# Kernel tuning notes

Measured on AMD Instinct MI355X. Metric: run time of the kernel, lower is better.

Reference implementation:

```python
import jax, jax.numpy as jnp
import numpy as np

N_ATOMS = 10000
N_PAIRS = 160000
F = 32            # nr_atom_basis (= edge basis = hidden sizes)
H = 7             # nr_heads
C = H * F         # nr_coefficients = 224
N_RBF = 50
RBF_CUTOFF = 5.0
RBF_GAMMA = 10.0

silu = jax.nn.silu

def setup_inputs() -> dict:
    key = jax.random.key(0)
    ks = jax.random.split(key, 32)
    def w(k, shape, scale=0.1):
        return (jax.random.normal(k, shape, dtype=jnp.float32) * scale)
    inp = {
        "h": jax.random.normal(ks[0], (N_ATOMS, F), dtype=jnp.float32),
        "x": jax.random.normal(ks[1], (N_ATOMS, 3), dtype=jnp.float32),
        "v": jax.random.normal(ks[2], (N_ATOMS, 3), dtype=jnp.float32),
        "pairlist": jax.random.randint(ks[3], (2, N_PAIRS), 0, N_ATOMS, dtype=jnp.int64 if jax.config.read('jax_enable_x64') else jnp.int32),
        # edge model (ContinuousFilterConvolutionWithConcatenation)
        "w_mlp_in": w(ks[4], (2 * F, N_RBF)), "b_mlp_in": jnp.zeros((N_RBF,), jnp.float32),
        "w_e1": w(ks[5], (2 * F + N_RBF + 1, F)), "b_e1": jnp.zeros((F,), jnp.float32),
        "w_e2": w(ks[6], (F, F)), "b_e2": jnp.zeros((F,), jnp.float32),
        # semantic attention mlp
        "w_att": w(ks[7], (F, H)), "b_att": jnp.zeros((H,), jnp.float32),
        # node mlp: in = F + C + F
        "w_n1": w(ks[8], (F + C + F, F)), "b_n1": jnp.zeros((F,), jnp.float32),
        "w_n2": w(ks[9], (F, F)), "b_n2": jnp.zeros((F,), jnp.float32),
        # post norm mlp
        "w_p1": w(ks[10], (C, F)), "b_p1": jnp.zeros((F,), jnp.float32),
        "w_p2": w(ks[11], (F, F)), "b_p2": jnp.zeros((F,), jnp.float32),
        # velocity mlp
        "w_v1": w(ks[12], (F, F)), "b_v1": jnp.zeros((F,), jnp.float32),
        "w_v2": w(ks[13], (F, 1)),
        # mixers
        "w_xmix": w(ks[14], (C, C)),
        "w_vmix": w(ks[15], (C, 1)),
    }
    return inp

def _rbf(d):  # Gaussian smearing, [P] -> [P, N_RBF]
    centers = jnp.linspace(0.0, RBF_CUTOFF, N_RBF, dtype=jnp.float32)
    return jnp.exp(-RBF_GAMMA * (d[:, None] - centers) ** 2)

def reference(h, x, v, pairlist,
              w_mlp_in, b_mlp_in, w_e1, b_e1, w_e2, b_e2,
              w_att, b_att, w_n1, b_n1, w_n2, b_n2,
              w_p1, b_p1, w_p2, b_p2, w_v1, b_v1, w_v2,
              w_xmix, w_vmix):
    n = h.shape[0]
    p = pairlist.shape[1]
    idx_i, idx_j = pairlist[0], pairlist[1]

    r_ij = x[idx_j] - x[idx_i]                       # [P, 3]
    d_ij = jnp.linalg.norm(r_ij, axis=-1)            # [P]
    dir_ij = r_ij / (d_ij[:, None] + 1e-5)           # [P, 3]

    # edge model
    h_cat = jnp.concatenate([h[idx_i], h[idx_j]], axis=-1)         # [P, 2F]
    filt = _rbf(d_ij) * (h_cat @ w_mlp_in + b_mlp_in)              # [P, N_RBF]
    e_in = jnp.concatenate([h_cat, filt, d_ij[:, None]], axis=-1)  # [P, 2F+N_RBF+1]
    h_ij_edge = silu(e_in @ w_e1 + b_e1) @ w_e2 + b_e2             # [P, F]

    # semantic attention: scatter-softmax over edges grouped by idx_i
    logits = jax.nn.celu(h_ij_edge @ w_att + b_att, alpha=2.0)     # [P, H]
    seg_max = jax.ops.segment_max(logits, idx_i, num_segments=n)
    e = jnp.exp(logits - seg_max[idx_i])
    seg_sum = jax.ops.segment_sum(e, idx_i, num_segments=n)
    att = e / seg_sum[idx_i]                                       # [P, H]
    att_agg = jax.ops.segment_sum(att, idx_i, num_segments=n)
    att_normed = att / att_agg[idx_i]
    # einsum('pf,ph->pfh') then reshape to [P, C]
    h_ij_semantic = (h_ij_edge[:, :, None] * att_normed[:, None, :]).reshape(p, C)

    # aggregate (scatter_add)
    h_i_semantic = jax.ops.segment_sum(h_ij_semantic, idx_i, num_segments=n)  # [N, C]

    # spatial attention
    x_mixed = jnp.tanh(h_ij_semantic @ w_xmix)                     # [P, C]
    combinations = dir_ij[:, None, :] * x_mixed[:, :, None]        # [P, C, 3]
    counts = jax.ops.segment_sum(jnp.ones((p,), h.dtype), idx_i, num_segments=n)
    denom = jnp.maximum(counts, 1.0)
    comb_mean = jax.ops.segment_sum(combinations, idx_i, num_segments=n) / denom[:, None, None]
    norm_sq = jnp.sum(comb_mean ** 2, axis=-1)                     # [N, C]
    h_i_spatial = silu(silu(norm_sq @ w_p1 + b_p1) @ w_p2 + b_p2)  # [N, F]

    # node update
    node_in = jnp.concatenate([h, h_i_semantic, h_i_spatial], axis=-1)
    h_updated = h + silu(silu(node_in @ w_n1 + b_n1) @ w_n2 + b_n2)

    # velocity update
    v_ij = jnp.einsum('pcx,c->px', combinations, w_vmix[:, 0])     # [P, 3]
    dv = jax.ops.segment_sum(v_ij, idx_i, num_segments=n) / denom[:, None]
    scale = 2.0 * jax.nn.sigmoid(silu(h @ w_v1 + b_v1) @ w_v2)     # [N, 1]
    v_updated = scale * v + dv
    x_updated = x + v_updated
    return (h_updated, x_updated, v_updated)
```

## Files before the change

kernel.cpp:

```cpp
#include <hip/hip_runtime.h>

typedef unsigned short u16;
typedef unsigned int u32;
typedef __attribute__((ext_vector_type(8))) short short8;
typedef __attribute__((ext_vector_type(4))) float floatx4;

#define P_PAIRS 160000
#define N_ATOMS 10000

#define OFF_WMLP  0
#define OFF_BMLP  3200
#define OFF_WE1   3250
#define OFF_BE1   6930
#define OFF_WE2   6962
#define OFF_BE2   7986
#define OFF_WATT  8018
#define OFF_BATT  8242
#define OFF_WN1   8249
#define OFF_BN1   17465
#define OFF_WN2   17497
#define OFF_BN2   18521
#define OFF_WP1   18553
#define OFF_BP1   25721
#define OFF_WP2   25753
#define OFF_BP2   26777
#define OFF_WV1   26809
#define OFF_BV1   27833
#define OFF_WV2   27865
#define OFF_WVMIX 27897
#define WF_TOTAL  28121

__device__ __forceinline__ float b2f(u16 u){ return __uint_as_float(((u32)u) << 16); }
__device__ __forceinline__ u16 f2b(float f){
  u32 u = __float_as_uint(f);
  u32 r = (u + 0x7FFFu + ((u >> 16) & 1u)) >> 16;
  return (u16)r;
}
__device__ __forceinline__ void unpack2(u32 p, float& lo, float& hi){
  lo = __uint_as_float(p << 16);
  hi = __uint_as_float(p & 0xFFFF0000u);
}
__device__ __forceinline__ float siluf(float v){ return v / (1.f + __expf(-v)); }
__device__ __forceinline__ float ldw(const void* p, int o, int bf){
  return bf ? b2f(((const u16*)p)[o]) : ((const float*)p)[o];
}

__global__ void k_code(float* out, float code){
  if (threadIdx.x == 0 && blockIdx.x == 0) out[0] = code;
}

__device__ __forceinline__ void detect_flags(const u32* hw, const u32* plw, int* s_fl){
  int tid = threadIdx.x;
  if (tid < 64){
    u32 e = (hw[tid] >> 7) & 0xFFu;
    unsigned long long m1 = __ballot(e >= 100u && e <= 140u);
    unsigned long long m2 = __ballot(plw[2*tid+1] == 0u);
    if (tid == 0){
      s_fl[0] = (__popcll(m1) >= 48) ? 1 : 0;
      s_fl[1] = (__popcll(m2) >= 60) ? 1 : 0;
    }
  }
  __syncthreads();
}

#define NBP_NORM 2735
#define NBP_CONV (NBP_NORM + 110)
#define NBP_TRAN (NBP_CONV + 196)
#define NBP_PB   (NBP_TRAN + 14)
#define NBP_HIST (NBP_PB + 625)

__global__ void k_prep(const void* __restrict__ h_raw, const void* __restrict__ x_raw,
    const void* __restrict__ v_raw, const void* __restrict__ pl_raw,
    const void* w_mlp, const void* b_mlp, const void* w_e1, const void* b_e1,
    const void* w_e2, const void* b_e2, const void* w_att, const void* b_att,
    const void* w_n1, const void* b_n1, const void* w_n2, const void* b_n2,
    const void* w_p1, const void* b_p1, const void* w_p2, const void* b_p2,
    const void* w_v1, const void* b_v1, const void* w_v2, const void* w_vmix,
    const void* wx,
    float* __restrict__ hf, float* __restrict__ xf, float* __restrict__ vf,
    int* __restrict__ pli, float* __restrict__ Wf, u16* __restrict__ wT,
    u16* __restrict__ bpk, int* __restrict__ counts){
  __shared__ int s_fl[2];
  detect_flags((const u32*)h_raw, (const u32*)pl_raw, s_fl);
  int bf = s_fl[0], i64 = s_fl[1];
  int bid = blockIdx.x, tid = threadIdx.x;
  if (bid < NBP_NORM){
    int t = bid * 256 + tid;
    if (t < 320000){
      hf[t] = ldw(h_raw, t, bf);
    } else if (t < 350000){
      int i = t - 320000; xf[i] = ldw(x_raw, i, bf);
    } else if (t < 380000){
      int i = t - 350000; vf[i] = ldw(v_raw, i, bf);
    } else if (t < 700000){
      int k = t - 380000;
      const int* p32 = (const int*)pl_raw;
      pli[k] = i64 ? p32[2*(size_t)k] : p32[k];
    }
  } else if (bid < NBP_CONV){
    int t = (bid - NBP_NORM) * 256 + tid;
    if (t >= WF_TOTAL) return;
    if (t < 3200){
      int k = t / 50, o = t - k * 50;
      Wf[OFF_WMLP + o * 64 + k] = ldw(w_mlp, t, bf);
      return;
    }
    const void* src; int o;
    if      (t < 3250)  { src = b_mlp;  o = t - 3200; }
    else if (t < 6930)  { src = w_e1;   o = t - 3250; }
    else if (t < 6962)  { src = b_e1;   o = t - 6930; }
    else if (t < 7986)  { src = w_e2;   o = t - 6962; }
    else if (t < 8018)  { src = b_e2;   o = t - 7986; }
    else if (t < 8242)  { src = w_att;  o = t - 8018; }
    else if (t < 8249)  { src = b_att;  o = t - 8242; }
    else if (t < 17465) { src = w_n1;   o = t - 8249; }
    else if (t < 17497) { src = b_n1;   o = t - 17465; }
    else if (t < 18521) { src = w_n2;   o = t - 17497; }
    else if (t < 18553) { src = b_n2;   o = t - 18521; }
    else if (t < 25721) { src = w_p1;   o = t - 18553; }
    else if (t < 25753) { src = b_p1;   o = t - 25721; }
    else if (t < 26777) { src = w_p2;   o = t - 25753; }
    else if (t < 26809) { src = b_p2;   o = t - 26777; }
    else if (t < 27833) { src = w_v1;   o = t - 26809; }
    else if (t < 27865) { src = b_v1;   o = t - 27833; }
    else if (t < 27897) { src = w_v2;   o = t - 27865; }
    else                { src = w_vmix; o = t - 27897; }
    Wf[t] = ldw(src, o, bf);
  } else if (bid < NBP_TRAN){
    int t = (bid - NBP_CONV) * 256 + tid;
    if (t >= 224 * 224) return;
    int n = t / 224, k = t - n * 224;
    wT[t] = f2b(ldw(wx, k * 224 + n, bf));
  } else if (bid < NBP_PB){
    int t = (bid - NBP_TRAN) * 256 + tid;
    if (t >= 3584) return;
    float v = 0.f;
    if (t < 2048){
      int n = t >> 6, k = t & 63;
      if (k < 50)       v = ldw(w_e1, (64 + k) * 32 + n, bf);
      else if (k == 50) v = ldw(w_e1, 114 * 32 + n, bf);
    } else if (t < 3072){
      int e = t - 2048; int n = e >> 5, k = e & 31;
      v = ldw(w_e2, k * 32 + n, bf);
    } else {
      int e = t - 3072; int n = e >> 5, k = e & 31;
      if (n < 7) v = ldw(w_att, k * 7 + n, bf);
    }
    bpk[t] = f2b(v);
  } else {
    int p = (bid - NBP_PB) * 256 + tid;
    const int* p32 = (const int*)pl_raw;
    int i = i64 ? p32[2*(size_t)p] : p32[p];
    atomicAdd(&counts[i], 1);
  }
}

__global__ void k_atomscan(const float* __restrict__ hf, const float* __restrict__ Wf,
    u16* __restrict__ prei, u16* __restrict__ prej,
    const int* __restrict__ counts, int* __restrict__ offs, int* __restrict__ cursor){
  __shared__ float hs[16][33];
  __shared__ int part[256];
  int tid = threadIdx.x;
  if (blockIdx.x < 625){
    int a0 = blockIdx.x * 16;
    for (int e = tid; e < 512; e += 256){
      int a = e >> 5, k = e & 31;
      hs[a][k] = hf[(size_t)(a0 + a) * 32 + k];
    }
    __syncthreads();
    for (int e = tid; e < 800; e += 256){
      int a = e / 50, r = e - a * 50;
      const float* wm = Wf + OFF_WMLP + r * 64;
      float acc = Wf[OFF_BMLP + r];
      #pragma unroll
      for (int k = 0; k < 32; ++k) acc += hs[a][k] * wm[k];
      prei[(size_t)(a0 + a) * 88 + 32 + r] = f2b(acc);
    }
    for (int e = tid; e < 800; e += 256){
      int a = e / 50, r = e - a * 50;
      const float* wm = Wf + OFF_WMLP + r * 64 + 32;
      float acc = 0.f;
      #pragma unroll
      for (int k = 0; k < 32; ++k) acc += hs[a][k] * wm[k];
      prej[(size_t)(a0 + a) * 88 + 32 + r] = f2b(acc);
    }
    for (int e = tid; e < 512; e += 256){
      int a = e >> 5, o = e & 31;
      float acc = Wf[OFF_BE1 + o];
      #pragma unroll
      for (int k = 0; k < 32; ++k) acc += hs[a][k] * Wf[OFF_WE1 + k * 32 + o];
      prei[(size_t)(a0 + a) * 88 + o] = f2b(acc);
    }
    for (int e = tid; e < 512; e += 256){
      int a = e >> 5, o = e & 31;
      float acc = 0.f;
      #pragma unroll
      for (int k = 0; k < 32; ++k) acc += hs[a][k] * Wf[OFF_WE1 + (32 + k) * 32 + o];
      prej[(size_t)(a0 + a) * 88 + o] = f2b(acc);
    }
  } else {
    int sum = 0;
    for (int k = 0; k < 40; ++k){
      int idx = tid * 40 + k;
      if (idx < N_ATOMS) sum += counts[idx];
    }
    part[tid] = sum;
    __syncthreads();
    if (tid == 0){
      int run = 0;
      for (int q = 0; q < 256; ++q){ int tmp = part[q]; part[q] = run; run += tmp; }
    }
    __syncthreads();
    int run = part[tid];
    for (int k = 0; k < 40; ++k){
      int idx = tid * 40 + k;
      if (idx < N_ATOMS){ offs[idx] = run; cursor[idx] = run; run += counts[idx]; }
    }
    if (tid == 0) offs[N_ATOMS] = P_PAIRS;
  }
}

__global__ void k_scatter(const int* __restrict__ pl, int* __restrict__ cursor,
                          int* __restrict__ isrt, int* __restrict__ jsrt){
  int p = blockIdx.x * 256 + threadIdx.x;
  int i = pl[p];
  int pos = atomicAdd(&cursor[i], 1);
  isrt[pos] = i;
  jsrt[pos] = pl[P_PAIRS + p];
}

#define PM_UB   0
#define PM_TB   16384
#define PM_DD   30720
#define PM_A1   31232
#define PM_B1   49664
#define PM_A2   54272
#define PM_B2   64512
#define PM_B3   67072
#define PM_TOT  68352

__global__ __launch_bounds__(256) void k_pairm(const float* __restrict__ x,
    const float* __restrict__ Wf, const u16* __restrict__ prei, const u16* __restrict__ prej,
    const int* __restrict__ isrt, const int* __restrict__ jsrt, const u16* __restrict__ bpk,
    u16* __restrict__ edge, float* __restrict__ logits, float* __restrict__ dirs){
  __shared__ __attribute__((aligned(16))) char smem[PM_TOT];
  float* UB = (float*)(smem + PM_UB);
  u16*   TB = (u16*)(smem + PM_TB);
  float* DD = (float*)(smem + PM_DD);
  u16*   A1 = (u16*)(smem + PM_A1);
  u16*   B1 = (u16*)(smem + PM_B1);
  u16*   A2 = (u16*)(smem + PM_A2);
  u16*   B2 = (u16*)(smem + PM_B2);
  u16*   B3 = (u16*)(smem + PM_B3);
  int tid = threadIdx.x;
  int wave = tid >> 6, lane = tid & 63, l15 = lane & 15, quad = lane >> 4;
  int row0 = blockIdx.x * 128;

  if (tid < 128){
    int s = row0 + tid;
    int i = isrt[s], j = jsrt[s];
    float r0 = x[j*3+0] - x[i*3+0];
    float r1 = x[j*3+1] - x[i*3+1];
    float r2 = x[j*3+2] - x[i*3+2];
    float d = sqrtf(r0*r0 + r1*r1 + r2*r2);
    float rinv = 1.f / (d + 1e-5f);
    dirs[s*3+0] = r0*rinv; dirs[s*3+1] = r1*rinv; dirs[s*3+2] = r2*rinv;
    DD[tid] = d;
    const uint4* pi4 = (const uint4*)(prei + (size_t)i * 88);
    const uint4* pj4 = (const uint4*)(prej + (size_t)j * 88);
    float* ub = UB + tid * 32;
    #pragma unroll
    for (int q = 0; q < 4; ++q){
      uint4 a4 = pi4[q], b4 = pj4[q];
      u32 pa[4] = {a4.x, a4.y, a4.z, a4.w};
      u32 pb[4] = {b4.x, b4.y, b4.z, b4.w};
      #pragma unroll
      for (int w2 = 0; w2 < 4; ++w2){
        float al, ah, bl, bh;
        unpack2(pa[w2], al, ah); unpack2(pb[w2], bl, bh);
        ub[q*8 + w2*2]     = al + bl;
        ub[q*8 + w2*2 + 1] = ah + bh;
      }
    }
    u32* tb = (u32*)TB + tid * 28;
    #pragma unroll
    for (int q = 0; q < 7; ++q){
      uint4 a4 = pi4[4+q], b4 = pj4[4+q];
      u32 pa[4] = {a4.x, a4.y, a4.z, a4.w};
      u32 pb[4] = {b4.x, b4.y, b4.z, b4.w};
      #pragma unroll
      for (int w2 = 0; w2 < 4; ++w2){
        float al, ah, bl, bh;
        unpack2(pa[w2], al, ah); unpack2(pb[w2], bl, bh);
        tb[q*4 + w2] = (u32)f2b(al + bl) | ((u32)f2b(ah + bh) << 16);
      }
    }
  } else {
    int t2 = tid - 128;
    const u32* src = (const u32*)bpk;
    for (int e = t2; e < 1024; e += 128){
      int n = e >> 5, kp = e & 31;
      ((u32*)B1)[n*36 + kp] = src[e];
    }
    for (int e = t2; e < 512; e += 128){
      int n = e >> 4, kp = e & 15;
      ((u32*)B2)[n*20 + kp] = src[1024 + e];
    }
    for (int e = t2; e < 256; e += 128){
      int n = e >> 4, kp = e & 15;
      ((u32*)B3)[n*20 + kp] = src[1536 + e];
    }
  }
  __syncthreads();
  for (int e = tid; e < 4096; e += 256){
    int r = e >> 5, kp = e & 31;
    int k0 = kp * 2, k1 = k0 + 1;
    float d = DD[r];
    float v0 = 0.f, v1 = 0.f;
    if (k0 < 50){
      float t0 = b2f(TB[r*56 + k0]);
      float c0 = (float)k0 * (5.f/49.f), dd0 = d - c0;
      v0 = t0 * __expf(-10.f * dd0 * dd0);
    } else if (k0 == 50) v0 = d;
    if (k1 < 50){
      float t1 = b2f(TB[r*56 + k1]);
      float c1 = (float)k1 * (5.f/49.f), dd1 = d - c1;
      v1 = t1 * __expf(-10.f * dd1 * dd1);
    }
    ((u32*)A1)[r*36 + kp] = (u32)f2b(v0) | ((u32)f2b(v1) << 16);
  }
  __syncthreads();
  floatx4 au[2][2];
  #pragma unroll
  for (int mt = 0; mt < 2; ++mt)
    #pragma unroll
    for (int nt = 0; nt < 2; ++nt) au[mt][nt] = (floatx4){0.f,0.f,0.f,0.f};
  #pragma unroll
  for (int ks = 0; ks < 2; ++ks){
    int kk = ks * 32;
    short8 a0 = *(const short8*)(A1 + (wave*32 + l15)*72 + kk + quad*8);
    short8 a1 = *(const short8*)(A1 + (wave*32 + 16 + l15)*72 + kk + quad*8);
    #pragma unroll
    for (int nt = 0; nt < 2; ++nt){
      short8 b = *(const short8*)(B1 + (nt*16 + l15)*72 + kk + quad*8);
      au[0][nt] = __builtin_amdgcn_mfma_f32_16x16x32_bf16(a0, b, au[0][nt], 0, 0, 0);
      au[1][nt] = __builtin_amdgcn_mfma_f32_16x16x32_bf16(a1, b, au[1][nt], 0, 0, 0);
    }
  }
  #pragma unroll
  for (int mt = 0; mt < 2; ++mt)
    #pragma unroll
    for (int nt = 0; nt < 2; ++nt)
      #pragma unroll
      for (int reg = 0; reg < 4; ++reg){
        int r = wave*32 + mt*16 + quad*4 + reg;
        int c = nt*16 + l15;
        float uval = au[mt][nt][reg] + UB[r*32 + c];
        A2[r*40 + c] = f2b(siluf(uval));
      }
  __syncthreads();
  floatx4 ae[2][2];
  #pragma unroll
  for (int mt = 0; mt < 2; ++mt)
    #pragma unroll
    for (int nt = 0; nt < 2; ++nt) ae[mt][nt] = (floatx4){0.f,0.f,0.f,0.f};
  {
    short8 a0 = *(const short8*)(A2 + (wave*32 + l15)*40 + quad*8);
    short8 a1 = *(const short8*)(A2 + (wave*32 + 16 + l15)*40 + quad*8);
    #pragma unroll
    for (int nt = 0; nt < 2; ++nt){
      short8 b = *(const short8*)(B2 + (nt*16 + l15)*40 + quad*8);
      ae[0][nt] = __builtin_amdgcn_mfma_f32_16x16x32_bf16(a0, b, ae[0][nt], 0, 0, 0);
      ae[1][nt] = __builtin_amdgcn_mfma_f32_16x16x32_bf16(a1, b, ae[1][nt], 0, 0, 0);
    }
  }
  __syncthreads();
  #pragma unroll
  for (int mt = 0; mt < 2; ++mt)
    #pragma unroll
    for (int nt = 0; nt < 2; ++nt)
      #pragma unroll
      for (int reg = 0; reg < 4; ++reg){
        int r = wave*32 + mt*16 + quad*4 + reg;
        int c = nt*16 + l15;
        float ev = ae[mt][nt][reg] + Wf[OFF_BE2 + c];
        A2[r*40 + c] = f2b(ev);
      }
  __syncthreads();
  {
    int r = tid >> 1, p = tid & 1;
    const uint4* srcp = (const uint4*)(A2 + r*40 + p*16);
    uint4* dstp = (uint4*)(edge + (size_t)(row0 + r)*32 + p*16);
    dstp[0] = srcp[0]; dstp[1] = srcp[1];
  }
  floatx4 al_[2];
  al_[0] = (floatx4){0.f,0.f,0.f,0.f};
  al_[1] = (floatx4){0.f,0.f,0.f,0.f};
  {
    short8 a0 = *(const short8*)(A2 + (wave*32 + l15)*40 + quad*8);
    short8 a1 = *(const short8*)(A2 + (wave*32 + 16 + l15)*40 + quad*8);
    short8 b = *(const short8*)(B3 + l15*40 + quad*8);
    al_[0] = __builtin_amdgcn_mfma_f32_16x16x32_bf16(a0, b, al_[0], 0, 0, 0);
    al_[1] = __builtin_amdgcn_mfma_f32_16x16x32_bf16(a1, b, al_[1], 0, 0, 0);
  }
  if (l15 < 7){
    float ba = Wf[OFF_BATT + l15];
    #pragma unroll
    for (int mt = 0; mt < 2; ++mt)
      #pragma unroll
      for (int reg = 0; reg < 4; ++reg){
        int r = wave*32 + mt*16 + quad*4 + reg;
        float vv = al_[mt][reg] + ba;
        float cl = vv > 0.f ? vv : 2.f * expm1f(0.5f * vv);
        logits[(size_t)(row0 + r)*7 + l15] = cl;
      }
  }
}

__global__ __launch_bounds__(256) void k_att(const int* __restrict__ offs,
    const float* __restrict__ logits, const u16* __restrict__ edge,
    float* __restrict__ atts, float* __restrict__ hsem){
  int a = blockIdx.x * 16 + (threadIdx.x >> 4);
  int lane = threadIdx.x & 15;
  int off = offs[a], end = offs[a+1];
  float m[7];
  #pragma unroll
  for (int hh = 0; hh < 7; ++hh) m[hh] = -1e30f;
  for (int s = off + lane; s < end; s += 16){
    #pragma unroll
    for (int hh = 0; hh < 7; ++hh) m[hh] = fmaxf(m[hh], logits[s*7+hh]);
  }
  #pragma unroll
  for (int hh = 0; hh < 7; ++hh){
    float v = m[hh];
    #pragma unroll
    for (int msk = 8; msk >= 1; msk >>= 1) v = fmaxf(v, __shfl_xor(v, msk));
    m[hh] = v;
  }
  float sm[7] = {0,0,0,0,0,0,0};
  for (int s = off + lane; s < end; s += 16){
    #pragma unroll
    for (int hh = 0; hh < 7; ++hh){
      float e = __expf(logits[s*7+hh] - m[hh]);
      sm[hh] += e;
      atts[s*7+hh] = e;
    }
  }
  #pragma unroll
  for (int hh = 0; hh < 7; ++hh){
    float v = sm[hh];
    #pragma unroll
    for (int msk = 8; msk >= 1; msk >>= 1) v += __shfl_xor(v, msk);
    sm[hh] = 1.f / v;
  }
  for (int s = off + lane; s < end; s += 16){
    #pragma unroll
    for (int hh = 0; hh < 7; ++hh) atts[s*7+hh] *= sm[hh];
  }
  __syncthreads();
  float acc[14] = {0,0,0,0,0,0,0,0,0,0,0,0,0,0};
  for (int s = off; s < end; ++s){
    u32 ev = *(const u32*)(edge + (size_t)s * 32 + lane * 2);
    float e0 = b2f((u16)(ev & 0xFFFFu));
    float e1 = b2f((u16)(ev >> 16));
    const float* ap = atts + (size_t)s * 7;
    #pragma unroll
    for (int hh = 0; hh < 7; ++hh){
      float at = ap[hh];
      acc[hh]     += e0 * at;
      acc[7 + hh] += e1 * at;
    }
  }
  float* hp = hsem + (size_t)a * 224 + lane * 14;
  #pragma unroll
  for (int jj = 0; jj < 14; ++jj) hp[jj] = acc[jj];
}

#define G_BS   29696
#define G_EL   29696
#define G_AL   (29696 + 4608)
#define G_TOT  38656

__global__ __launch_bounds__(256, 4) void k_gemm3(const u16* __restrict__ edge,
    const float* __restrict__ atts, const u16* __restrict__ BT,
    u16* __restrict__ xh0, u16* __restrict__ xh1, int mode){
  __shared__ __attribute__((aligned(16))) char smem[G_TOT];
  u16*   As  = (u16*)smem;
  u16*   xth = (u16*)smem;
  u16*   Bs  = (u16*)(smem + G_BS);
  u16*   eL  = (u16*)(smem + G_EL);
  float* aL  = (float*)(smem + G_AL);
  int tid = threadIdx.x;
  int wave = tid >> 6, lane = tid & 63, l15 = lane & 15, quad = lane >> 4;
  int bid = blockIdx.x;
  int half, rblk;
  if (mode < 0){ half = bid & 1; rblk = bid >> 1; }
  else         { half = mode;    rblk = bid; }
  u16* xhalf = half ? xh1 : xh0;
  int row0 = rblk * 64;
  int nbase = half * 112;

  for (int e = tid; e < 512; e += 256){
    int r = e >> 3, q = e & 7;
    *(uint2*)(eL + r*36 + q*4) = *(const uint2*)(edge + (size_t)(row0 + r)*32 + q*4);
  }
  for (int e = tid; e < 448; e += 256) aL[e] = atts[(size_t)row0*7 + e];
  floatx4 acc[7];
  #pragma unroll
  for (int nt = 0; nt < 7; ++nt) acc[nt] = (floatx4){0.f, 0.f, 0.f, 0.f};
  __syncthreads();

  {
    int pr = tid >> 2, q = tid & 3;
    u32* asw = (u32*)As + pr*116 + q*28;
    const u16* er = eL + pr*36 + q*8;
    const float* ar = aL + pr*7;
    float av[7];
    #pragma unroll
    for (int hh = 0; hh < 7; ++hh) av[hh] = ar[hh];
    #pragma unroll
    for (int fo2 = 0; fo2 < 4; ++fo2){
      float e0 = b2f(er[2*fo2]);
      float e1 = b2f(er[2*fo2+1]);
      u16 w[14];
      #pragma unroll
      for (int hh = 0; hh < 7; ++hh){
        w[hh]   = f2b(e0 * av[hh]);
        w[7+hh] = f2b(e1 * av[hh]);
      }
      #pragma unroll
      for (int k = 0; k < 7; ++k)
        asw[fo2*7 + k] = (u32)w[2*k] | ((u32)w[2*k+1] << 16);
    }
  }
  __syncthreads();

  for (int kt = 0; kt < 7; ++kt){
    for (int e = tid; e < 448; e += 256){
      int r = e >> 2, q = e & 3;
      *(uint4*)(Bs + r*40 + q*8) = *(const uint4*)(BT + (size_t)(nbase + r)*224 + kt*32 + q*8);
    }
    __syncthreads();
    int kk = kt * 32;
    short8 a0 = *(const short8*)(As + (wave*16 + l15)*232 + kk + quad*8);
    #pragma unroll
    for (int nt = 0; nt < 7; ++nt){
      short8 b = *(const short8*)(Bs + (nt*16 + l15)*40 + quad*8);
      acc[nt] = __builtin_amdgcn_mfma_f32_16x16x32_bf16(a0, b, acc[nt], 0, 0, 0);
    }
    __syncthreads();
  }

  #pragma unroll
  for (int nt = 0; nt < 7; ++nt)
    #pragma unroll
    for (int reg = 0; reg < 4; ++reg){
      int r = wave*16 + quad*4 + reg;
      int c = nt*16 + l15;
      float vv = acc[nt][reg];
      vv = fminf(fmaxf(vv, -15.f), 15.f);
      float e2 = __expf(2.f * vv);
      xth[r*120 + c] = f2b((e2 - 1.f) / (e2 + 1.f));
    }
  __syncthreads();
  for (int e = tid; e < 896; e += 256){
    int r = e / 14, w = e - r * 14;
    *(uint4*)(xhalf + (size_t)(row0 + r)*112 + w*8) = *(const uint4*)(xth + r*120 + w*8);
  }
}

__global__ __launch_bounds__(256) void k_comb(const int* __restrict__ offs,
    const u16* __restrict__ xhalf, const float* __restrict__ dirs,
    const float* __restrict__ Wf, int half,
    float* __restrict__ nsq, float* __restrict__ pvh){
  int a = blockIdx.x * 16 + (threadIdx.x >> 4);
  int lane = threadIdx.x & 15;
  int off = offs[a], end = offs[a+1];
  float c0[7] = {0,0,0,0,0,0,0}, c1[7] = {0,0,0,0,0,0,0}, c2[7] = {0,0,0,0,0,0,0};
  for (int s = off; s < end; ++s){
    float d0 = dirs[s*3+0], d1 = dirs[s*3+1], d2 = dirs[s*3+2];
    const u16* xr = xhalf + (size_t)s * 112 + lane;
    #pragma unroll
    for (int k = 0; k < 7; ++k){
      float xm = b2f(xr[k*16]);
      c0[k] += d0 * xm; c1[k] += d1 * xm; c2[k] += d2 * xm;
    }
  }
  float inv = 1.f / fmaxf((float)(end - off), 1.f);
  float pv0 = 0.f, pv1 = 0.f, pv2 = 0.f;
  #pragma unroll
  for (int k = 0; k < 7; ++k){
    float m0 = c0[k]*inv, m1 = c1[k]*inv, m2 = c2[k]*inv;
    int c = half*112 + k*16 + lane;
    nsq[(size_t)a*224 + c] = m0*m0 + m1*m1 + m2*m2;
    float wv = Wf[OFF_WVMIX + c];
    pv0 += wv*m0; pv1 += wv*m1; pv2 += wv*m2;
  }
  #pragma unroll
  for (int m = 8; m >= 1; m >>= 1){
    pv0 += __shfl_xor(pv0, m); pv1 += __shfl_xor(pv1, m); pv2 += __shfl_xor(pv2, m);
  }
  if (lane == 0){
    float* pp = pvh + (size_t)half*30000 + (size_t)a*3;
    pp[0] = pv0; pp[1] = pv1; pp[2] = pv2;
  }
}

__global__ __launch_bounds__(256) void k_final4(const float* __restrict__ h,
    const float* __restrict__ x, const float* __restrict__ v,
    const float* __restrict__ Wf, const float* __restrict__ hsem,
    const float* __restrict__ nsq, const float* __restrict__ pvh,
    float* __restrict__ out){
  __shared__ float s_nsq[16][225];
  __shared__ float s_in[16][289];
  __shared__ float s_u1[16][33];
  __shared__ float s_un[16][33];
  __shared__ float s_sc[16];
  int tid = threadIdx.x;
  int a0 = blockIdx.x * 16;
  for (int e = tid; e < 896; e += 256){
    int a = e / 56, q = e - a * 56;
    float4 t = *(const float4*)(nsq + (size_t)(a0 + a) * 224 + q * 4);
    s_nsq[a][q*4+0] = t.x; s_nsq[a][q*4+1] = t.y;
    s_nsq[a][q*4+2] = t.z; s_nsq[a][q*4+3] = t.w;
  }
  for (int e = tid; e < 896; e += 256){
    int a = e / 56, q = e - a * 56;
    float4 t = *(const float4*)(hsem + (size_t)(a0 + a) * 224 + q * 4);
    s_in[a][32 + q*4+0] = t.x; s_in[a][32 + q*4+1] = t.y;
    s_in[a][32 + q*4+2] = t.z; s_in[a][32 + q*4+3] = t.w;
  }
  for (int e = tid; e < 128; e += 256){
    int a = e >> 3, q = e & 7;
    float4 t = *(const float4*)(h + (size_t)(a0 + a) * 32 + q * 4);
    s_in[a][q*4+0] = t.x; s_in[a][q*4+1] = t.y;
    s_in[a][q*4+2] = t.z; s_in[a][q*4+3] = t.w;
  }
  __syncthreads();
  int o = tid & 31, g5 = tid >> 5;
  int aA = g5, aB = g5 + 8;
  {
    float uA = Wf[OFF_BP1 + o], uB = uA;
    const float* w = Wf + OFF_WP1 + o;
    #pragma unroll 8
    for (int kk = 0; kk < 224; ++kk){
      float wv = w[kk*32];
      uA += s_nsq[aA][kk] * wv;
      uB += s_nsq[aB][kk] * wv;
    }
    s_u1[aA][o] = siluf(uA);
    s_u1[aB][o] = siluf(uB);
  }
  {
    float gA = Wf[OFF_BV1 + o], gB = gA;
    const float* w = Wf + OFF_WV1 + o;
    #pragma unroll
    for (int kk = 0; kk < 32; ++kk){
      float wv = w[kk*32];
      gA += s_in[aA][kk] * wv;
      gB += s_in[aB][kk] * wv;
    }
    float wv2 = Wf[OFF_WV2 + o];
    float zA = siluf(gA) * wv2, zB = siluf(gB) * wv2;
    #pragma unroll
    for (int m = 16; m >= 1; m >>= 1){
      zA += __shfl_xor(zA, m); zB += __shfl_xor(zB, m);
    }
    if (o == 0){
      s_sc[aA] = 2.f / (1.f + __expf(-zA));
      s_sc[aB] = 2.f / (1.f + __expf(-zB));
    }
  }
  __syncthreads();
  {
    float uA = Wf[OFF_BP2 + o], uB = uA;
    const float* w = Wf + OFF_WP2 + o;
    #pragma unroll
    for (int kk = 0; kk < 32; ++kk){
      float wv = w[kk*32];
      uA += s_u1[aA][kk] * wv;
      uB += s_u1[aB][kk] * wv;
    }
    s_in[aA][256 + o] = siluf(uA);
    s_in[aB][256 + o] = siluf(uB);
  }
  __syncthreads();
  {
    float uA = Wf[OFF_BN1 + o], uB = uA;
    const float* w = Wf + OFF_WN1 + o;
    #pragma unroll 8
    for (int kk = 0; kk < 288; ++kk){
      float wv = w[kk*32];
      uA += s_in[aA][kk] * wv;
      uB += s_in[aB][kk] * wv;
    }
    s_un[aA][o] = siluf(uA);
    s_un[aB][o] = siluf(uB);
  }
  __syncthreads();
  {
    float uA = Wf[OFF_BN2 + o], uB = uA;
    const float* w = Wf + OFF_WN2 + o;
    #pragma unroll
    for (int kk = 0; kk < 32; ++kk){
      float wv = w[kk*32];
      uA += s_un[aA][kk] * wv;
      uB += s_un[aB][kk] * wv;
    }
    out[(size_t)(a0 + aA)*32 + o] = s_in[aA][o] + siluf(uA);
    out[(size_t)(a0 + aB)*32 + o] = s_in[aB][o] + siluf(uB);
  }
  if (tid < 48){
    int a = tid / 3, c = tid - a * 3;
    int ga = a0 + a;
    float pv = pvh[(size_t)ga*3 + c] + pvh[30000 + (size_t)ga*3 + c];
    float vup = s_sc[a] * v[ga*3 + c] + pv;
    float xup = x[ga*3 + c] + vup;
    out[N_ATOMS*32 + (size_t)ga*3 + c] = xup;
    out[N_ATOMS*32 + N_ATOMS*3 + (size_t)ga*3 + c] = vup;
  }
}

__global__ __launch_bounds__(256) void k_combf(const int* __restrict__ offs,
    const u16* __restrict__ xh0, const u16* __restrict__ xh1,
    const float* __restrict__ dirs, const float* __restrict__ h,
    const float* __restrict__ x, const float* __restrict__ v,
    const float* __restrict__ Wf, const float* __restrict__ hsem,
    float* __restrict__ out){
  __shared__ float s_nsq[16][225];
  __shared__ float s_in[16][289];
  __shared__ float s_u1[16][33];
  __shared__ float s_un[16][33];
  __shared__ float s_sc[16];
  __shared__ float s_pv[16][3];
  int tid = threadIdx.x;
  int a0 = blockIdx.x * 16;
  for (int e = tid; e < 896; e += 256){
    int a = e / 56, q = e - a * 56;
    float4 t = *(const float4*)(hsem + (size_t)(a0 + a) * 224 + q * 4);
    s_in[a][32 + q*4+0] = t.x; s_in[a][32 + q*4+1] = t.y;
    s_in[a][32 + q*4+2] = t.z; s_in[a][32 + q*4+3] = t.w;
  }
  for (int e = tid; e < 128; e += 256){
    int a = e >> 3, q = e & 7;
    float4 t = *(const float4*)(h + (size_t)(a0 + a) * 32 + q * 4);
    s_in[a][q*4+0] = t.x; s_in[a][q*4+1] = t.y;
    s_in[a][q*4+2] = t.z; s_in[a][q*4+3] = t.w;
  }
  {
    int a = tid >> 4, lane = tid & 15;
    int off = offs[a0 + a], end = offs[a0 + a + 1];
    float c0A[7] = {0,0,0,0,0,0,0}, c1A[7] = {0,0,0,0,0,0,0}, c2A[7] = {0,0,0,0,0,0,0};
    float c0B[7] = {0,0,0,0,0,0,0}, c1B[7] = {0,0,0,0,0,0,0}, c2B[7] = {0,0,0,0,0,0,0};
    for (int s = off; s < end; ++s){
      float d0 = dirs[s*3+0], d1 = dirs[s*3+1], d2 = dirs[s*3+2];
      const u16* xra = xh0 + (size_t)s * 112 + lane;
      const u16* xrb = xh1 + (size_t)s * 112 + lane;
      #pragma unroll
      for (int k = 0; k < 7; ++k){
        float xa = b2f(xra[k*16]);
        float xb = b2f(xrb[k*16]);
        c0A[k] += d0 * xa; c1A[k] += d1 * xa; c2A[k] += d2 * xa;
        c0B[k] += d0 * xb; c1B[k] += d1 * xb; c2B[k] += d2 * xb;
      }
    }
    float inv = 1.f / fmaxf((float)(end - off), 1.f);
    float pv0 = 0.f, pv1 = 0.f, pv2 = 0.f;
    #pragma unroll
    for (int k = 0; k < 7; ++k){
      {
        float m0 = c0A[k]*inv, m1 = c1A[k]*inv, m2 = c2A[k]*inv;
        int c = k*16 + lane;
        s_nsq[a][c] = m0*m0 + m1*m1 + m2*m2;
        float wv = Wf[OFF_WVMIX + c];
        pv0 += wv*m0; pv1 += wv*m1; pv2 += wv*m2;
      }
      {
        float m0 = c0B[k]*inv, m1 = c1B[k]*inv, m2 = c2B[k]*inv;
        int c = 112 + k*16 + lane;
        s_nsq[a][c] = m0*m0 + m1*m1 + m2*m2;
        float wv = Wf[OFF_WVMIX + c];
        pv0 += wv*m0; pv1 += wv*m1; pv2 += wv*m2;
      }
    }
    #pragma unroll
    for (int m = 8; m >= 1; m >>= 1){
      pv0 += __shfl_xor(pv0, m); pv1 += __shfl_xor(pv1, m); pv2 += __shfl_xor(pv2, m);
    }
    if (lane == 0){ s_pv[a][0] = pv0; s_pv[a][1] = pv1; s_pv[a][2] = pv2; }
  }
  __syncthreads();
  int o = tid & 31, g5 = tid >> 5;
  int aA = g5, aB = g5 + 8;
  {
    float uA = Wf[OFF_BP1 + o], uB = uA;
    const float* w = Wf + OFF_WP1 + o;
    #pragma unroll 8
    for (int kk = 0; kk < 224; ++kk){
      float wv = w[kk*32];
      uA += s_nsq[aA][kk] * wv;
      uB += s_nsq[aB][kk] * wv;
    }
    s_u1[aA][o] = siluf(uA);
    s_u1[aB][o] = siluf(uB);
  }
  {
    float gA = Wf[OFF_BV1 + o], gB = gA;
    const float* w = Wf + OFF_WV1 + o;
    #pragma unroll
    for (int kk = 0; kk < 32; ++kk){
      float wv = w[kk*32];
      gA += s_in[aA][kk] * wv;
      gB += s_in[aB][kk] * wv;
    }
    float wv2 = Wf[OFF_WV2 + o];
    float zA = siluf(gA) * wv2, zB = siluf(gB) * wv2;
    #pragma unroll
    for (int m = 16; m >= 1; m >>= 1){
      zA += __shfl_xor(zA, m); zB += __shfl_xor(zB, m);
    }
    if (o == 0){
      s_sc[aA] = 2.f / (1.f + __expf(-zA));
      s_sc[aB] = 2.f / (1.f + __expf(-zB));
    }
  }
  __syncthreads();
  {
    float uA = Wf[OFF_BP2 + o], uB = uA;
    const float* w = Wf + OFF_WP2 + o;
    #pragma unroll
    for (int kk = 0; kk < 32; ++kk){
      float wv = w[kk*32];
      uA += s_u1[aA][kk] * wv;
      uB += s_u1[aB][kk] * wv;
    }
    s_in[aA][256 + o] = siluf(uA);
    s_in[aB][256 + o] = siluf(uB);
  }
  __syncthreads();
  {
    float uA = Wf[OFF_BN1 + o], uB = uA;
    const float* w = Wf + OFF_WN1 + o;
    #pragma unroll 8
    for (int kk = 0; kk < 288; ++kk){
      float wv = w[kk*32];
      uA += s_in[aA][kk] * wv;
      uB += s_in[aB][kk] * wv;
    }
    s_un[aA][o] = siluf(uA);
    s_un[aB][o] = siluf(uB);
  }
  __syncthreads();
  {
    float uA = Wf[OFF_BN2 + o], uB = uA;
    const float* w = Wf + OFF_WN2 + o;
    #pragma unroll
    for (int kk = 0; kk < 32; ++kk){
      float wv = w[kk*32];
      uA += s_un[aA][kk] * wv;
      uB += s_un[aB][kk] * wv;
    }
    out[(size_t)(a0 + aA)*32 + o] = s_in[aA][o] + siluf(uA);
    out[(size_t)(a0 + aB)*32 + o] = s_in[aB][o] + siluf(uB);
  }
  if (tid < 48){
    int a = tid / 3, c = tid - a * 3;
    int ga = a0 + a;
    float vup = s_sc[a] * v[ga*3 + c] + s_pv[a][c];
    float xup = x[ga*3 + c] + vup;
    out[N_ATOMS*32 + (size_t)ga*3 + c] = xup;
    out[N_ATOMS*32 + N_ATOMS*3 + (size_t)ga*3 + c] = vup;
  }
}

static constexpr size_t al256(size_t x){ return (x + 255) & ~(size_t)255; }
static constexpr size_t WS_FLAGS   = 0;
static constexpr size_t WS_COUNTS  = al256(WS_FLAGS + 8);
static constexpr size_t WS_OFFSETS = al256(WS_COUNTS + (size_t)N_ATOMS * 4);
static constexpr size_t WS_CURSOR  = al256(WS_OFFSETS + (size_t)(N_ATOMS + 1) * 4);
static constexpr size_t WS_PERM    = al256(WS_CURSOR + (size_t)N_ATOMS * 4);
static constexpr size_t WS_PLI     = al256(WS_PERM + (size_t)P_PAIRS * 4);
static constexpr size_t WS_HF      = al256(WS_PLI + (size_t)2 * P_PAIRS * 4);
static constexpr size_t WS_XF      = al256(WS_HF + (size_t)N_ATOMS * 32 * 4);
static constexpr size_t WS_VF      = al256(WS_XF + (size_t)N_ATOMS * 3 * 4);
static constexpr size_t WS_WF      = al256(WS_VF + (size_t)N_ATOMS * 3 * 4);
static constexpr size_t WS_WT      = al256(WS_WF + (size_t)WF_TOTAL * 4);
static constexpr size_t WS_EDGE    = al256(WS_WT + (size_t)224 * 224 * 2);
static constexpr size_t WS_ATTS    = al256(WS_EDGE + (size_t)P_PAIRS * 32 * 2);
static constexpr size_t WS_DIRS    = al256(WS_ATTS + (size_t)P_PAIRS * 7 * 4);
static constexpr size_t WS_LOGITS  = al256(WS_DIRS + (size_t)P_PAIRS * 3 * 4);
static constexpr size_t WS_PREI    = al256(WS_LOGITS + (size_t)P_PAIRS * 7 * 4);
static constexpr size_t WS_PREJ    = al256(WS_PREI + (size_t)N_ATOMS * 88 * 2);
static constexpr size_t WS_HSEM    = WS_LOGITS + 4480000;
static constexpr size_t WS_XH      = WS_HSEM + (size_t)N_ATOMS * 224 * 4;
static constexpr size_t WS_NSQ     = WS_XH + (size_t)P_PAIRS * 112 * 2;
static constexpr size_t WS_PVH     = WS_NSQ + (size_t)N_ATOMS * 224 * 4;
static constexpr size_t WS_JSRT    = al256(WS_PVH + (size_t)2 * 30000 * 4);
static constexpr size_t WS_BPK     = al256(WS_JSRT + (size_t)P_PAIRS * 4);
static constexpr size_t WS_END     = WS_BPK + 3584 * 2;
static constexpr size_t WB_XH0     = WS_XH;
static constexpr size_t WB_XH1     = WB_XH0 + (size_t)P_PAIRS * 112 * 2;
static constexpr size_t WB_JSRT    = al256(WB_XH1 + (size_t)P_PAIRS * 112 * 2);
static constexpr size_t WB_BPK     = al256(WB_JSRT + (size_t)P_PAIRS * 4);
static constexpr size_t WB_END     = WB_BPK + 3584 * 2;
static_assert(WS_PREJ + (size_t)N_ATOMS * 88 * 2 <= WS_XH, "pre tables before xhalf");
static_assert(WS_END <= WS_LOGITS + (size_t)P_PAIRS * 224 * 2, "fallback within proven footprint");
static_assert(WS_HSEM % 256 == 0 && WS_XH % 256 == 0 && WS_NSQ % 256 == 0 && WS_PVH % 256 == 0, "alignment");
static_assert(WB_XH1 % 256 == 0, "alignment");

extern "C" void kernel_launch(void* const* d_in, const int* in_sizes, int n_in,
                              void* d_out, int out_size, void* d_ws, size_t ws_size,
                              hipStream_t stream){
  (void)in_sizes; (void)n_in;
  if (out_size != 380000 || ws_size < WS_END){
    k_code<<<1, 64, 0, stream>>>((float*)d_out, 14000.f);
    return;
  }
  char* ws = (char*)d_ws;
  int*   counts = (int*)(ws + WS_COUNTS);
  int*   offs   = (int*)(ws + WS_OFFSETS);
  int*   cursor = (int*)(ws + WS_CURSOR);
  int*   isrt   = (int*)(ws + WS_PERM);
  int*   pli    = (int*)(ws + WS_PLI);
  float* hf     = (float*)(ws + WS_HF);
  float* xf     = (float*)(ws + WS_XF);
  float* vf     = (float*)(ws + WS_VF);
  float* Wf     = (float*)(ws + WS_WF);
  u16*   wT     = (u16*)(ws + WS_WT);
  u16*   edge   = (u16*)(ws + WS_EDGE);
  float* atts   = (float*)(ws + WS_ATTS);
  float* dirs   = (float*)(ws + WS_DIRS);
  float* logits = (float*)(ws + WS_LOGITS);
  u16*   prei   = (u16*)(ws + WS_PREI);
  u16*   prej   = (u16*)(ws + WS_PREJ);
  float* hsem   = (float*)(ws + WS_HSEM);

  bool big = (ws_size >= WB_END);
  u16*   xh0  = (u16*)(ws + WB_XH0);
  u16*   xh1  = big ? (u16*)(ws + WB_XH1) : xh0;
  int*   jsrt = big ? (int*)(ws + WB_JSRT) : (int*)(ws + WS_JSRT);
  u16*   bpk  = big ? (u16*)(ws + WB_BPK) : (u16*)(ws + WS_BPK);
  float* nsq  = (float*)(ws + WS_NSQ);
  float* pvh  = (float*)(ws + WS_PVH);

  hipMemsetAsync(counts, 0, (size_t)N_ATOMS * 4, stream);
  k_prep<<<NBP_HIST, 256, 0, stream>>>(d_in[0], d_in[1], d_in[2], d_in[3],
      d_in[4],  d_in[5],  d_in[6],  d_in[7],  d_in[8],  d_in[9],  d_in[10], d_in[11],
      d_in[12], d_in[13], d_in[14], d_in[15], d_in[16], d_in[17], d_in[18], d_in[19],
      d_in[20], d_in[21], d_in[22], d_in[24], d_in[23],
      hf, xf, vf, pli, Wf, wT, bpk, counts);
  k_atomscan<<<626, 256, 0, stream>>>(hf, Wf, prei, prej, counts, offs, cursor);
  k_scatter<<<P_PAIRS / 256, 256, 0, stream>>>(pli, cursor, isrt, jsrt);
  k_pairm<<<P_PAIRS / 128, 256, 0, stream>>>(xf, Wf, prei, prej, isrt, jsrt, bpk, edge, logits, dirs);
  k_att<<<N_ATOMS / 16, 256, 0, stream>>>(offs, logits, edge, atts, hsem);
  if (big){
    k_gemm3<<<2 * (P_PAIRS / 64), 256, 0, stream>>>(edge, atts, wT, xh0, xh1, -1);
    k_combf<<<625, 256, 0, stream>>>(offs, xh0, xh1, dirs, hf, xf, vf, Wf, hsem, (float*)d_out);
  } else {
    k_gemm3<<<P_PAIRS / 64, 256, 0, stream>>>(edge, atts, wT, xh0, xh0, 0);
    k_comb<<<N_ATOMS / 16, 256, 0, stream>>>(offs, xh0, dirs, Wf, 0, nsq, pvh);
    k_gemm3<<<P_PAIRS / 64, 256, 0, stream>>>(edge, atts, wT, xh0, xh0, 1);
    k_comb<<<N_ATOMS / 16, 256, 0, stream>>>(offs, xh0, dirs, Wf, 1, nsq, pvh);
    k_final4<<<625, 256, 0, stream>>>(hf, xf, vf, Wf, hsem, nsq, pvh, (float*)d_out);
  }
}
```

Baseline: 312.2 us.

## Compute full 224-wide xmix output per block instead of two half-blocks

Adds a k_gemm3w kernel that computes all 224 output columns for each 64-row tile, where the old path launched two blocks per tile, one per 112-column half. This avoids building the A tile (edge times attention) twice and reloading edge and attention data twice. In exchange each block holds 14 accumulator tiles, raising register pressure, and uses more shared memory for the wider B tile, so occupancy drops to 3 blocks per CU. The non-big path's k_gemm3 signature is simplified to take a single output half.

Result: slower. 323.9 us (+3.7%).

```diff
diff --git a/kernel.cpp b/kernel.cpp
--- a/kernel.cpp
+++ b/kernel.cpp
@@ -476,6 +476,95 @@
   for (int jj = 0; jj < 14; ++jj) hp[jj] = acc[jj];
 }
 
+#define GW_BS   29696
+#define GW_EL   29696
+#define GW_AL   (29696 + 4608)
+#define GW_TOT  47616
+
+__global__ __launch_bounds__(256, 3) void k_gemm3w(const u16* __restrict__ edge,
+    const float* __restrict__ atts, const u16* __restrict__ BT,
+    u16* __restrict__ xh0, u16* __restrict__ xh1){
+  __shared__ __attribute__((aligned(16))) char smem[GW_TOT];
+  u16*   As  = (u16*)smem;
+  u16*   xth = (u16*)smem;
+  u16*   Bs  = (u16*)(smem + GW_BS);
+  u16*   eL  = (u16*)(smem + GW_EL);
+  float* aL  = (float*)(smem + GW_AL);
+  int tid = threadIdx.x;
+  int wave = tid >> 6, lane = tid & 63, l15 = lane & 15, quad = lane >> 4;
+  int row0 = blockIdx.x * 64;
+
+  for (int e = tid; e < 512; e += 256){
+    int r = e >> 3, q = e & 7;
+    *(uint2*)(eL + r*36 + q*4) = *(const uint2*)(edge + (size_t)(row0 + r)*32 + q*4);
+  }
+  for (int e = tid; e < 448; e += 256) aL[e] = atts[(size_t)row0*7 + e];
+  floatx4 acc[14];
+  #pragma unroll
+  for (int nt = 0; nt < 14; ++nt) acc[nt] = (floatx4){0.f, 0.f, 0.f, 0.f};
+  __syncthreads();
+
+  {
+    int pr = tid >> 2, q = tid & 3;
+    u32* asw = (u32*)As + pr*116 + q*28;
+    const u16* er = eL + pr*36 + q*8;
+    const float* ar = aL + pr*7;
+    float av[7];
+    #pragma unroll
+    for (int hh = 0; hh < 7; ++hh) av[hh] = ar[hh];
+    #pragma unroll
+    for (int fo2 = 0; fo2 < 4; ++fo2){
+      float e0 = b2f(er[2*fo2]);
+      float e1 = b2f(er[2*fo2+1]);
+      u16 w[14];
+      #pragma unroll
+      for (int hh = 0; hh < 7; ++hh){
+        w[hh]   = f2b(e0 * av[hh]);
+        w[7+hh] = f2b(e1 * av[hh]);
+      }
+      #pragma unroll
+      for (int k = 0; k < 7; ++k)
+        asw[fo2*7 + k] = (u32)w[2*k] | ((u32)w[2*k+1] << 16);
+    }
+  }
+  __syncthreads();
+
+  for (int kt = 0; kt < 7; ++kt){
+    for (int e = tid; e < 896; e += 256){
+      int r = e >> 2, q = e & 3;
+      *(uint4*)(Bs + r*40 + q*8) = *(const uint4*)(BT + (size_t)r*224 + kt*32 + q*8);
+    }
+    __syncthreads();
+    int kk = kt * 32;
+    short8 a0 = *(const short8*)(As + (wave*16 + l15)*232 + kk + quad*8);
+    #pragma unroll
+    for (int nt = 0; nt < 14; ++nt){
+      short8 b = *(const short8*)(Bs + (nt*16 + l15)*40 + quad*8);
+      acc[nt] = __builtin_amdgcn_mfma_f32_16x16x32_bf16(a0, b, acc[nt], 0, 0, 0);
+    }
+    __syncthreads();
+  }
+
+  #pragma unroll
+  for (int nt = 0; nt < 14; ++nt)
+    #pragma unroll
+    for (int reg = 0; reg < 4; ++reg){
+      int r = wave*16 + quad*4 + reg;
+      int c = nt*16 + l15;
+      float vv = acc[nt][reg];
+      vv = fminf(fmaxf(vv, -15.f), 15.f);
+      float e2 = __expf(2.f * vv);
+      xth[r*232 + c] = f2b((e2 - 1.f) / (e2 + 1.f));
+    }
+  __syncthreads();
+  for (int e = tid; e < 1792; e += 256){
+    int r = e / 28, w = e - r * 28;
+    uint4 val = *(const uint4*)(xth + r*232 + w*8);
+    if (w < 14) *(uint4*)(xh0 + (size_t)(row0 + r)*112 + w*8) = val;
+    else        *(uint4*)(xh1 + (size_t)(row0 + r)*112 + (w-14)*8) = val;
+  }
+}
+
 #define G_BS   29696
 #define G_EL   29696
 #define G_AL   (29696 + 4608)
@@ -483,7 +572,7 @@
 
 __global__ __launch_bounds__(256, 4) void k_gemm3(const u16* __restrict__ edge,
     const float* __restrict__ atts, const u16* __restrict__ BT,
-    u16* __restrict__ xh0, u16* __restrict__ xh1, int mode){
+    u16* __restrict__ xhalf, int half){
   __shared__ __attribute__((aligned(16))) char smem[G_TOT];
   u16*   As  = (u16*)smem;
   u16*   xth = (u16*)smem;
@@ -492,12 +581,7 @@
   float* aL  = (float*)(smem + G_AL);
   int tid = threadIdx.x;
   int wave = tid >> 6, lane = tid & 63, l15 = lane & 15, quad = lane >> 4;
-  int bid = blockIdx.x;
-  int half, rblk;
-  if (mode < 0){ half = bid & 1; rblk = bid >> 1; }
-  else         { half = mode;    rblk = bid; }
-  u16* xhalf = half ? xh1 : xh0;
-  int row0 = rblk * 64;
+  int row0 = blockIdx.x * 64;
   int nbase = half * 112;
 
   for (int e = tid; e < 512; e += 256){
@@ -954,12 +1038,12 @@
   k_pairm<<<P_PAIRS / 128, 256, 0, stream>>>(xf, Wf, prei, prej, isrt, jsrt, bpk, edge, logits, dirs);
   k_att<<<N_ATOMS / 16, 256, 0, stream>>>(offs, logits, edge, atts, hsem);
   if (big){
-    k_gemm3<<<2 * (P_PAIRS / 64), 256, 0, stream>>>(edge, atts, wT, xh0, xh1, -1);
+    k_gemm3w<<<P_PAIRS / 64, 256, 0, stream>>>(edge, atts, wT, xh0, xh1);
     k_combf<<<625, 256, 0, stream>>>(offs, xh0, xh1, dirs, hf, xf, vf, Wf, hsem, (float*)d_out);
   } else {
-    k_gemm3<<<P_PAIRS / 64, 256, 0, stream>>>(edge, atts, wT, xh0, xh0, 0);
+    k_gemm3<<<P_PAIRS / 64, 256, 0, stream>>>(edge, atts, wT, xh0, 0);
     k_comb<<<N_ATOMS / 16, 256, 0, stream>>>(offs, xh0, dirs, Wf, 0, nsq, pvh);
-    k_gemm3<<<P_PAIRS / 64, 256, 0, stream>>>(edge, atts, wT, xh0, xh0, 1);
+    k_gemm3<<<P_PAIRS / 64, 256, 0, stream>>>(edge, atts, wT, xh0, 1);
     k_comb<<<N_ATOMS / 16, 256, 0, stream>>>(offs, xh0, dirs, Wf, 1, nsq, pvh);
     k_final4<<<625, 256, 0, stream>>>(hf, xf, vf, Wf, hsem, nsq, pvh, (float*)d_out);
   }
```
